# Optimization experiments

Measured on AMD Instinct MI355X. Metric: run time of the kernel, lower is better.

The kernel has to match this reference:

```python
import jax, jax.numpy as jnp
import numpy as np
from jax import lax

# Conv3d(in_dim, in_dim, kernel=(1,3,3), padding=(0,1,1)) == per-time-slice 3x3 conv mixing channels

def _conv3d(x, w, b):
    # x: [B, C, T, W, H], w: [O, I, 1, 3, 3], b: [O]
    y = lax.conv_general_dilated(
        x, w,
        window_strides=(1, 1, 1),
        padding=[(0, 0), (1, 1), (1, 1)],
        dimension_numbers=("NCDHW", "OIDHW", "NCDHW"),
    )
    return y + b[None, :, None, None, None]


def setup_inputs() -> dict:
    key = jax.random.key(0)
    ks = jax.random.split(key, 8)
    B, C, T, W, H = 8, 64, 16, 64, 64
    fan = C * 1 * 3 * 3
    bound = 1.0 / np.sqrt(fan)  # torch Conv3d default init range
    x = jax.random.normal(ks[0], (B, C, T, W, H), dtype=jnp.float32)
    wq = jax.random.uniform(ks[1], (C, C, 1, 3, 3), jnp.float32, -bound, bound)
    wk = jax.random.uniform(ks[2], (C, C, 1, 3, 3), jnp.float32, -bound, bound)
    wv = jax.random.uniform(ks[3], (C, C, 1, 3, 3), jnp.float32, -bound, bound)
    bq = jax.random.uniform(ks[4], (C,), jnp.float32, -bound, bound)
    bk = jax.random.uniform(ks[5], (C,), jnp.float32, -bound, bound)
    bv = jax.random.uniform(ks[6], (C,), jnp.float32, -bound, bound)
    # torch init is gamma=0 (identity output); use nonzero so reference exercises the full path
    gamma = jax.random.normal(ks[7], (1,), dtype=jnp.float32) * 0.1
    return {"x": x, "wq": wq, "wk": wk, "wv": wv,
            "bq": bq, "bk": bk, "bv": bv, "gamma": gamma}


def reference(x, wq, wk, wv, bq, bk, bv, gamma):
    B, C, T, W, H = x.shape
    WH = W * H
    q = _conv3d(x, wq, bq).reshape(B, C, T, WH)
    k = _conv3d(x, wk, bk).reshape(B, C, T, WH)
    v = _conv3d(x, wv, bv).reshape(B, C, T, WH)
    # Original: (q[...,:,None] @ k[...,None,:]) @ v[...,:,None]  -> rank-1 energy, no softmax.
    # Exact reassociation: out_i = q_i * sum_j(k_j * v_j), avoiding the [WH, WH] matrix.
    s = jnp.sum(k * v, axis=-1, keepdims=True)  # [B, C, T, 1]
    out = (q * s).reshape(B, C, T, W, H)
    return gamma[0] * out + x
```

## Files before the change

### kernel.cpp

```cpp
#include <hip/hip_runtime.h>
#include <hip/hip_bf16.h>
#include <stdint.h>

typedef __attribute__((ext_vector_type(8))) short bf16x8;
typedef __attribute__((ext_vector_type(4))) float f32x4v;
typedef __attribute__((ext_vector_type(16))) float f32x16;

#define CH_STRIDE 65536

__device__ __forceinline__ uint16_t f2bf(float f) {
  uint32_t u = __builtin_bit_cast(uint32_t, f);
  u = (u + 0x7FFFu + ((u >> 16) & 1u)) >> 16;
  return (uint16_t)u;
}
__device__ __forceinline__ float bf2f(uint32_t b) {
  return __builtin_bit_cast(float, b << 16);
}
__device__ __forceinline__ uint16_t cvt_bf(float f) {
  return __builtin_bit_cast(uint16_t, __float2bfloat16(f));
}

#define MFMA32(a, b, c) __builtin_amdgcn_mfma_f32_32x32x16_bf16(a, b, c, 0, 0, 0)
#define LGKM0 asm volatile("s_waitcnt lgkmcnt(0)" ::: "memory")
#define BAR __builtin_amdgcn_s_barrier()
#define SCHED0 __builtin_amdgcn_sched_barrier(0)

#define LDSX6  (6 * 8 * 66 * 16)
#define LDSX10 (10 * 8 * 66 * 16)

__device__ __forceinline__ uint32_t swz(uint32_t b) {
  return b ^ (((b >> 7) & 7u) << 4);
}

__device__ __forceinline__ bf16x8 ldx(const uint8_t* ldsx, int row, int oct, int ci) {
  return *(const bf16x8*)(ldsx + swz((uint32_t)((row * 8 + oct) * 66 + ci) * 16u));
}

__device__ __forceinline__ void stage_unit(uint8_t* ldsx, const float* xs, int w0, int u) {
  int row = u >> 7, oct = (u >> 4) & 7, g = u & 15;
  int w = w0 - 1 + row;
  uint32_t base = (uint32_t)((row * 8 + oct) * 66 + 4 * g + 1) * 16u;
  if ((unsigned)w < 64u) {
    const float* p = xs + (size_t)(oct * 8) * CH_STRIDE + w * 64 + 4 * g;
    f32x4v v[8];
    #pragma unroll
    for (int j = 0; j < 8; ++j) v[j] = *(const f32x4v*)(p + (size_t)j * CH_STRIDE);
    #pragma unroll
    for (int c = 0; c < 4; ++c) {
      bf16x8 frag;
      #pragma unroll
      for (int q = 0; q < 4; ++q) {
        frag[2 * q]     = (short)cvt_bf(v[2 * q][c]);
        frag[2 * q + 1] = (short)cvt_bf(v[2 * q + 1][c]);
      }
      *(bf16x8*)(ldsx + swz(base + (uint32_t)c * 16u)) = frag;
    }
  } else {
    bf16x8 z = {};
    #pragma unroll
    for (int c = 0; c < 4; ++c)
      *(bf16x8*)(ldsx + swz(base + (uint32_t)c * 16u)) = z;
  }
}
__device__ __forceinline__ void stage_halo(uint8_t* ldsx, int tid, int nrow) {
  if (tid < nrow * 16) {
    int row = tid >> 4, rem = tid & 15;
    int oct = rem >> 1, side = rem & 1;
    bf16x8 z = {};
    *(bf16x8*)(ldsx + swz((uint32_t)((row * 8 + oct) * 66 + side * 65) * 16u)) = z;
  }
}
__device__ __forceinline__ void stage_x256(uint8_t* ldsx, const float* xs, int w0, int tid) {
  stage_halo(ldsx, tid, 6);
  #pragma unroll
  for (int k = 0; k < 3; ++k) stage_unit(ldsx, xs, w0, tid + k * 256);
}
__device__ __forceinline__ void stage_x1024(uint8_t* ldsx, const float* xs, int w0, int tid) {
  stage_halo(ldsx, tid, 10);
  stage_unit(ldsx, xs, w0, tid);
  if (tid < 256) stage_unit(ldsx, xs, w0, 1024 + tid);
}

__device__ __forceinline__ bf16x8 ldw_kv(const uint8_t* ldsw, int oct, int rowloc) {
  return *(const bf16x8*)(ldsw + (uint32_t)(oct * 128 + rowloc) * 16u);
}
__device__ __forceinline__ bf16x8 ldw_q(const uint8_t* ldsw, int oct, int row) {
  return *(const bf16x8*)(ldsw + (uint32_t)(oct * 64 + row) * 16u);
}
__device__ __forceinline__ void ldw_g_q(bf16x8* r, const uint16_t* wq, int tap, int tid) {
  #pragma unroll
  for (int k = 0; k < 2; ++k)
    r[k] = *(const bf16x8*)(wq + ((size_t)tap * 512 + tid + k * 256) * 8);
}
__device__ __forceinline__ void stw_q(uint8_t* ldsw, const bf16x8* r, int tid) {
  #pragma unroll
  for (int k = 0; k < 2; ++k)
    *(bf16x8*)(ldsw + (uint32_t)(tid + k * 256) * 16u) = r[k];
}

__global__ void prep_weights(const float* __restrict__ wq, const float* __restrict__ wk,
                             const float* __restrict__ wv, uint16_t* __restrict__ wout) {
  int i = blockIdx.x * 256 + threadIdx.x;
  if (i >= 110592) return;
  if (i < 36864) {
    int tap = i >> 12, oct = (i >> 9) & 7, row = (i >> 3) & 63, j = i & 7;
    wout[i] = f2bf(wq[(row * 64 + oct * 8 + j) * 9 + tap]);
  } else {
    int m = i - 36864;
    int tap = m >> 13, oct = (m >> 10) & 7, rl = (m >> 3) & 127, j = m & 7;
    const float* src = (rl < 64) ? wk : wv;
    wout[i] = f2bf(src[((rl & 63) * 64 + oct * 8 + j) * 9 + tap]);
  }
}

__global__ __launch_bounds__(1024, 4) void kv_s_kernel(
    const float* __restrict__ x, const uint16_t* __restrict__ wkv,
    const float* __restrict__ bk, const float* __restrict__ bv,
    float* __restrict__ s_out) {
  extern __shared__ uint8_t lds[];
  uint8_t* ldsx = lds;
  uint8_t* ldswA = lds + LDSX10;
  uint8_t* ldswB = lds + LDSX10 + 16384;
  const int tid = threadIdx.x;
  const int l = tid & 63;
  const int wid = tid >> 6;
  const int ng = wid & 7, mg = wid >> 3;
  int bid = (int)(blockIdx.x & 7) * 128 + (int)(blockIdx.x >> 3);
  const int rg = bid & 7, slice = bid >> 3;
  const int b = slice >> 4, t = slice & 15;
  const int w0 = rg * 8;
  const float* xs = x + ((size_t)b * 1024 + t) * 4096;
  const int lm = l & 31, lh = l >> 5;

  stage_x1024(ldsx, xs, w0, tid);
  bf16x8 r_pref;
  r_pref = *(const bf16x8*)(wkv + (size_t)tid * 8);
  *(bf16x8*)(ldswA + (uint32_t)tid * 16u) = r_pref;
  r_pref = *(const bf16x8*)(wkv + ((size_t)1024 + tid) * 8);
  SCHED0; LGKM0; BAR; SCHED0;

  f32x16 accK[2], accV[2];
  #pragma unroll
  for (int nt = 0; nt < 2; ++nt)
    #pragma unroll
    for (int q = 0; q < 16; ++q) { accK[nt][q] = 0.f; accV[nt][q] = 0.f; }

  #pragma unroll
  for (int tap = 0; tap < 9; ++tap) {
    const int dy = tap / 3, dx = tap % 3;
    const uint8_t* bufc = (tap & 1) ? ldswB : ldswA;
    uint8_t* bufn = (tap & 1) ? ldswA : ldswB;
    int oct0 = lh;
    bf16x8 aK = ldw_kv(bufc, oct0, mg * 32 + lm);
    bf16x8 aV = ldw_kv(bufc, oct0, 64 + mg * 32 + lm);
    bf16x8 b0 = ldx(ldsx, ng + dy, oct0, lm + dx);
    bf16x8 b1 = ldx(ldsx, ng + dy, oct0, 32 + lm + dx);
    if (tap < 8) {
      *(bf16x8*)(bufn + (uint32_t)tid * 16u) = r_pref;
      if (tap < 7)
        r_pref = *(const bf16x8*)(wkv + ((size_t)(tap + 2) * 1024 + tid) * 8);
    }
    __builtin_amdgcn_s_setprio(1);
    accK[0] = MFMA32(aK, b0, accK[0]);
    accK[1] = MFMA32(aK, b1, accK[1]);
    accV[0] = MFMA32(aV, b0, accV[0]);
    accV[1] = MFMA32(aV, b1, accV[1]);
    #pragma unroll
    for (int s = 1; s < 4; ++s) {
      int oct = s * 2 + lh;
      aK = ldw_kv(bufc, oct, mg * 32 + lm);
      aV = ldw_kv(bufc, oct, 64 + mg * 32 + lm);
      b0 = ldx(ldsx, ng + dy, oct, lm + dx);
      b1 = ldx(ldsx, ng + dy, oct, 32 + lm + dx);
      accK[0] = MFMA32(aK, b0, accK[0]);
      accK[1] = MFMA32(aK, b1, accK[1]);
      accV[0] = MFMA32(aV, b0, accV[0]);
      accV[1] = MFMA32(aV, b1, accV[1]);
    }
    __builtin_amdgcn_s_setprio(0);
    SCHED0; LGKM0; BAR; SCHED0;
  }

  __syncthreads();
  float* red = (float*)lds;
  #pragma unroll
  for (int q = 0; q < 16; ++q) {
    int cl = (q & 3) + 8 * (q >> 2) + 4 * lh;
    int c = mg * 32 + cl;
    float bkc = bk[c], bvc = bv[c];
    float p = (accK[0][q] + bkc) * (accV[0][q] + bvc)
            + (accK[1][q] + bkc) * (accV[1][q] + bvc);
    red[c * 260 + ng * 32 + lm] = p;
  }
  __syncthreads();
  if (tid < 64) {
    const f32x4v* rp = (const f32x4v*)(red + tid * 260);
    f32x4v a4 = {0.f, 0.f, 0.f, 0.f};
    #pragma unroll
    for (int j = 0; j < 64; ++j) a4 += rp[j];
    atomicAdd(s_out + (b * 16 + t) * 64 + tid, a4[0] + a4[1] + a4[2] + a4[3]);
  }
}

__global__ __launch_bounds__(256, 2) void q_out_kernel(
    const float* __restrict__ x, const uint16_t* __restrict__ wq,
    const float* __restrict__ bq, const float* __restrict__ s_in,
    const float* __restrict__ gamma, float* __restrict__ out) {
  extern __shared__ uint8_t lds[];
  uint8_t* ldsx = lds;
  uint8_t* ldsw = lds + LDSX6;
  const int tid = threadIdx.x;
  const int l = tid & 63, ng = tid >> 6;
  int bid = (int)(blockIdx.x & 7) * 256 + (int)(blockIdx.x >> 3);
  const int rg = bid & 15, slice = bid >> 4;
  const int b = slice >> 4, t = slice & 15;
  const int w0 = rg * 4;
  const float* xs = x + ((size_t)b * 1024 + t) * 4096;
  const int lm = l & 31, lh = l >> 5;

  stage_x256(ldsx, xs, w0, tid);
  bf16x8 r[2];
  ldw_g_q(r, wq, 0, tid);
  stw_q(ldsw, r, tid);
  ldw_g_q(r, wq, 1, tid);
  SCHED0; LGKM0; BAR; SCHED0;

  f32x16 acc[2][2];
  #pragma unroll
  for (int mt = 0; mt < 2; ++mt)
    #pragma unroll
    for (int nt = 0; nt < 2; ++nt)
      #pragma unroll
      for (int q = 0; q < 16; ++q) acc[mt][nt][q] = 0.f;

  #pragma unroll
  for (int tap = 0; tap < 9; ++tap) {
    const int dy = tap / 3, dx = tap % 3;
    __builtin_amdgcn_s_setprio(1);
    #pragma unroll
    for (int s = 0; s < 4; ++s) {
      int oct = s * 2 + lh;
      bf16x8 a0 = ldw_q(ldsw, oct, lm);
      bf16x8 a1 = ldw_q(ldsw, oct, 32 + lm);
      bf16x8 b0 = ldx(ldsx, ng + dy, oct, lm + dx);
      bf16x8 b1 = ldx(ldsx, ng + dy, oct, 32 + lm + dx);
      acc[0][0] = MFMA32(a0, b0, acc[0][0]);
      acc[0][1] = MFMA32(a0, b1, acc[0][1]);
      acc[1][0] = MFMA32(a1, b0, acc[1][0]);
      acc[1][1] = MFMA32(a1, b1, acc[1][1]);
    }
    __builtin_amdgcn_s_setprio(0);
    if (tap < 8) {
      SCHED0; BAR;
      stw_q(ldsw, r, tid);
      if (tap < 7) ldw_g_q(r, wq, tap + 2, tid);
      SCHED0; LGKM0; BAR; SCHED0;
    }
  }

  float g = gamma[0];
  const float* sb = s_in + (b * 16 + t) * 64;
  int w = w0 + ng;
  #pragma unroll
  for (int mt = 0; mt < 2; ++mt) {
    #pragma unroll
    for (int q = 0; q < 16; ++q) {
      int cl = (q & 3) + 8 * (q >> 2) + 4 * lh;
      int c  = mt * 32 + cl;
      float qb = bq[c], sc = sb[c];
      #pragma unroll
      for (int nt = 0; nt < 2; ++nt) {
        int h = nt * 32 + lm;
        uint32_t xb = (uint32_t)(((ng + 1) * 8 + (c >> 3)) * 66 + (h + 1)) * 16u
                    + (uint32_t)(c & 7) * 2u;
        float xv = bf2f(*(const uint16_t*)(ldsx + swz(xb)));
        size_t idx = ((size_t)(b * 64 + c) * 16 + t) * 4096 + (size_t)w * 64 + h;
        out[idx] = g * (acc[mt][nt][q] + qb) * sc + xv;
      }
    }
  }
}

extern "C" void kernel_launch(void* const* d_in, const int* in_sizes, int n_in,
                              void* d_out, int out_size, void* d_ws, size_t ws_size,
                              hipStream_t stream) {
  const float* x   = (const float*)d_in[0];
  const float* wq  = (const float*)d_in[1];
  const float* wk  = (const float*)d_in[2];
  const float* wv  = (const float*)d_in[3];
  const float* bq  = (const float*)d_in[4];
  const float* bk  = (const float*)d_in[5];
  const float* bv  = (const float*)d_in[6];
  const float* gam = (const float*)d_in[7];

  uint16_t* wbf = (uint16_t*)d_ws;
  float* sbuf   = (float*)((uint8_t*)d_ws + 221184);

  hipMemsetAsync(sbuf, 0, 8 * 16 * 64 * sizeof(float), stream);
  prep_weights<<<(110592 + 255) / 256, 256, 0, stream>>>(wq, wk, wv, wbf);
  kv_s_kernel<<<1024, 1024, LDSX10 + 32768, stream>>>(x, wbf + 36864, bk, bv, sbuf);
  q_out_kernel<<<2048, 256, LDSX6 + 8192, stream>>>(x, wbf, bq, sbuf, gam, (float*)d_out);
}
```

Before: 156.2 us.

## Pre-transpose x into padded bf16 channel-interleaved layout shared by both conv kernels

Adds a transpose_x kernel that converts x once into a bf16, halo-padded, channel-octet-interleaved layout in workspace. Both the KV and Q conv kernels then stage their input tiles with straight 16-byte copies instead of each doing strided fp32 loads and bf16 conversion, which halves the bytes they read and removes duplicated conversion work. The LDS swizzle is dropped because the staged layout is now a linear copy, and the reduction stride changes to 261. The cost is an extra pass that writes and rereads a roughly 71 MB buffer, plus possible LDS bank conflicts now that there is no swizzle.

```diff
diff --git a/kernel.cpp b/kernel.cpp
--- a/kernel.cpp
+++ b/kernel.cpp
@@ -7,6 +7,8 @@
 typedef __attribute__((ext_vector_type(16))) float f32x16;
 
 #define CH_STRIDE 65536
+#define ROW_B 8448
+#define SLICE_B 557568
 
 __device__ __forceinline__ uint16_t f2bf(float f) {
   uint32_t u = __builtin_bit_cast(uint32_t, f);
@@ -28,57 +30,8 @@
 #define LDSX6  (6 * 8 * 66 * 16)
 #define LDSX10 (10 * 8 * 66 * 16)
 
-__device__ __forceinline__ uint32_t swz(uint32_t b) {
-  return b ^ (((b >> 7) & 7u) << 4);
-}
-
 __device__ __forceinline__ bf16x8 ldx(const uint8_t* ldsx, int row, int oct, int ci) {
-  return *(const bf16x8*)(ldsx + swz((uint32_t)((row * 8 + oct) * 66 + ci) * 16u));
-}
-
-__device__ __forceinline__ void stage_unit(uint8_t* ldsx, const float* xs, int w0, int u) {
-  int row = u >> 7, oct = (u >> 4) & 7, g = u & 15;
-  int w = w0 - 1 + row;
-  uint32_t base = (uint32_t)((row * 8 + oct) * 66 + 4 * g + 1) * 16u;
-  if ((unsigned)w < 64u) {
-    const float* p = xs + (size_t)(oct * 8) * CH_STRIDE + w * 64 + 4 * g;
-    f32x4v v[8];
-    #pragma unroll
-    for (int j = 0; j < 8; ++j) v[j] = *(const f32x4v*)(p + (size_t)j * CH_STRIDE);
-    #pragma unroll
-    for (int c = 0; c < 4; ++c) {
-      bf16x8 frag;
-      #pragma unroll
-      for (int q = 0; q < 4; ++q) {
-        frag[2 * q]     = (short)cvt_bf(v[2 * q][c]);
-        frag[2 * q + 1] = (short)cvt_bf(v[2 * q + 1][c]);
-      }
-      *(bf16x8*)(ldsx + swz(base + (uint32_t)c * 16u)) = frag;
-    }
-  } else {
-    bf16x8 z = {};
-    #pragma unroll
-    for (int c = 0; c < 4; ++c)
-      *(bf16x8*)(ldsx + swz(base + (uint32_t)c * 16u)) = z;
-  }
-}
-__device__ __forceinline__ void stage_halo(uint8_t* ldsx, int tid, int nrow) {
-  if (tid < nrow * 16) {
-    int row = tid >> 4, rem = tid & 15;
-    int oct = rem >> 1, side = rem & 1;
-    bf16x8 z = {};
-    *(bf16x8*)(ldsx + swz((uint32_t)((row * 8 + oct) * 66 + side * 65) * 16u)) = z;
-  }
-}
-__device__ __forceinline__ void stage_x256(uint8_t* ldsx, const float* xs, int w0, int tid) {
-  stage_halo(ldsx, tid, 6);
-  #pragma unroll
-  for (int k = 0; k < 3; ++k) stage_unit(ldsx, xs, w0, tid + k * 256);
-}
-__device__ __forceinline__ void stage_x1024(uint8_t* ldsx, const float* xs, int w0, int tid) {
-  stage_halo(ldsx, tid, 10);
-  stage_unit(ldsx, xs, w0, tid);
-  if (tid < 256) stage_unit(ldsx, xs, w0, 1024 + tid);
+  return *(const bf16x8*)(ldsx + (uint32_t)((row * 8 + oct) * 66 + ci) * 16u);
 }
 
 __device__ __forceinline__ bf16x8 ldw_kv(const uint8_t* ldsw, int oct, int rowloc) {
@@ -113,8 +66,61 @@
   }
 }
 
+__global__ __launch_bounds__(256, 4) void transpose_x(const float* __restrict__ x,
+                                                      uint8_t* __restrict__ xT) {
+  __shared__ uint8_t lds[4 * 8 * 66 * 16];
+  const int tid = threadIdx.x;
+  const int bid = blockIdx.x;
+  const int gg = bid % 17, slice = bid / 17;
+  const int b = slice >> 4, t = slice & 15;
+  const int r0 = gg * 4;
+  const int nrow = (gg == 16) ? 2 : 4;
+  const float* xs = x + ((size_t)b * 1024 + t) * 4096;
+
+  if (tid < nrow * 16) {
+    int row = tid >> 4, rem = tid & 15;
+    int oct = rem >> 1, side = rem & 1;
+    bf16x8 z = {};
+    *(bf16x8*)(lds + (uint32_t)((row * 8 + oct) * 66 + side * 65) * 16u) = z;
+  }
+  #pragma unroll
+  for (int k = 0; k < 2; ++k) {
+    int u = tid + k * 256;
+    if (u < nrow * 128) {
+      int row = u >> 7, oct = (u >> 4) & 7, g = u & 15;
+      int w = r0 + row - 1;
+      uint32_t base = (uint32_t)((row * 8 + oct) * 66 + 4 * g + 1) * 16u;
+      if ((unsigned)w < 64u) {
+        const float* p = xs + (size_t)(oct * 8) * CH_STRIDE + w * 64 + 4 * g;
+        f32x4v v[8];
+        #pragma unroll
+        for (int j = 0; j < 8; ++j) v[j] = *(const f32x4v*)(p + (size_t)j * CH_STRIDE);
+        #pragma unroll
+        for (int c = 0; c < 4; ++c) {
+          bf16x8 frag;
+          #pragma unroll
+          for (int q = 0; q < 4; ++q) {
+            frag[2 * q]     = (short)cvt_bf(v[2 * q][c]);
+            frag[2 * q + 1] = (short)cvt_bf(v[2 * q + 1][c]);
+          }
+          *(bf16x8*)(lds + base + (uint32_t)c * 16u) = frag;
+        }
+      } else {
+        bf16x8 z = {};
+        #pragma unroll
+        for (int c = 0; c < 4; ++c)
+          *(bf16x8*)(lds + base + (uint32_t)c * 16u) = z;
+      }
+    }
+  }
+  __syncthreads();
+  uint8_t* dst = xT + (size_t)slice * SLICE_B + (size_t)r0 * 528 * 16;
+  for (int i = tid; i < nrow * 528; i += 256)
+    *(bf16x8*)(dst + (uint32_t)i * 16u) = *(const bf16x8*)(lds + (uint32_t)i * 16u);
+}
+
 __global__ __launch_bounds__(1024, 4) void kv_s_kernel(
-    const float* __restrict__ x, const uint16_t* __restrict__ wkv,
+    const uint8_t* __restrict__ xT, const uint16_t* __restrict__ wkv,
     const float* __restrict__ bk, const float* __restrict__ bv,
     float* __restrict__ s_out) {
   extern __shared__ uint8_t lds[];
@@ -129,10 +135,15 @@
   const int rg = bid & 7, slice = bid >> 3;
   const int b = slice >> 4, t = slice & 15;
   const int w0 = rg * 8;
-  const float* xs = x + ((size_t)b * 1024 + t) * 4096;
   const int lm = l & 31, lh = l >> 5;
 
-  stage_x1024(ldsx, xs, w0, tid);
+  const uint8_t* gx = xT + (size_t)slice * SLICE_B + (size_t)w0 * ROW_B;
+  #pragma unroll
+  for (int k = 0; k < 6; ++k) {
+    int idx = tid + k * 1024;
+    if (idx < 5280)
+      *(bf16x8*)(ldsx + (uint32_t)idx * 16u) = *(const bf16x8*)(gx + (uint32_t)idx * 16u);
+  }
   bf16x8 r_pref;
   r_pref = *(const bf16x8*)(wkv + (size_t)tid * 8);
   *(bf16x8*)(ldswA + (uint32_t)tid * 16u) = r_pref;
@@ -190,20 +201,20 @@
     float bkc = bk[c], bvc = bv[c];
     float p = (accK[0][q] + bkc) * (accV[0][q] + bvc)
             + (accK[1][q] + bkc) * (accV[1][q] + bvc);
-    red[c * 260 + ng * 32 + lm] = p;
+    red[c * 261 + ng * 32 + lm] = p;
   }
   __syncthreads();
   if (tid < 64) {
-    const f32x4v* rp = (const f32x4v*)(red + tid * 260);
+    const float* rp = red + tid * 261;
     f32x4v a4 = {0.f, 0.f, 0.f, 0.f};
     #pragma unroll
-    for (int j = 0; j < 64; ++j) a4 += rp[j];
+    for (int j = 0; j < 64; ++j) a4 += *(const f32x4v*)(rp + j * 4);
     atomicAdd(s_out + (b * 16 + t) * 64 + tid, a4[0] + a4[1] + a4[2] + a4[3]);
   }
 }
 
 __global__ __launch_bounds__(256, 2) void q_out_kernel(
-    const float* __restrict__ x, const uint16_t* __restrict__ wq,
+    const uint8_t* __restrict__ xT, const uint16_t* __restrict__ wq,
     const float* __restrict__ bq, const float* __restrict__ s_in,
     const float* __restrict__ gamma, float* __restrict__ out) {
   extern __shared__ uint8_t lds[];
@@ -215,10 +226,15 @@
   const int rg = bid & 15, slice = bid >> 4;
   const int b = slice >> 4, t = slice & 15;
   const int w0 = rg * 4;
-  const float* xs = x + ((size_t)b * 1024 + t) * 4096;
   const int lm = l & 31, lh = l >> 5;
 
-  stage_x256(ldsx, xs, w0, tid);
+  const uint8_t* gx = xT + (size_t)slice * SLICE_B + (size_t)w0 * ROW_B;
+  #pragma unroll
+  for (int k = 0; k < 13; ++k) {
+    int idx = tid + k * 256;
+    if (idx < 3168)
+      *(bf16x8*)(ldsx + (uint32_t)idx * 16u) = *(const bf16x8*)(gx + (uint32_t)idx * 16u);
+  }
   bf16x8 r[2];
   ldw_g_q(r, wq, 0, tid);
   stw_q(ldsw, r, tid);
@@ -273,7 +289,7 @@
         int h = nt * 32 + lm;
         uint32_t xb = (uint32_t)(((ng + 1) * 8 + (c >> 3)) * 66 + (h + 1)) * 16u
                     + (uint32_t)(c & 7) * 2u;
-        float xv = bf2f(*(const uint16_t*)(ldsx + swz(xb)));
+        float xv = bf2f(*(const uint16_t*)(ldsx + xb));
         size_t idx = ((size_t)(b * 64 + c) * 16 + t) * 4096 + (size_t)w * 64 + h;
         out[idx] = g * (acc[mt][nt][q] + qb) * sc + xv;
       }
@@ -295,9 +311,12 @@
 
   uint16_t* wbf = (uint16_t*)d_ws;
   float* sbuf   = (float*)((uint8_t*)d_ws + 221184);
+  uint8_t* xT   = (uint8_t*)d_ws + 1048576;
+  if (ws_size < (size_t)1048576 + 128 * (size_t)SLICE_B) return;
 
   hipMemsetAsync(sbuf, 0, 8 * 16 * 64 * sizeof(float), stream);
   prep_weights<<<(110592 + 255) / 256, 256, 0, stream>>>(wq, wk, wv, wbf);
-  kv_s_kernel<<<1024, 1024, LDSX10 + 32768, stream>>>(x, wbf + 36864, bk, bv, sbuf);
-  q_out_kernel<<<2048, 256, LDSX6 + 8192, stream>>>(x, wbf, bq, sbuf, gam, (float*)d_out);
-}
+  transpose_x<<<128 * 17, 256, 0, stream>>>(x, xT);
+  kv_s_kernel<<<1024, 1024, LDSX10 + 32768, stream>>>(xT, wbf + 36864, bk, bv, sbuf);
+  q_out_kernel<<<2048, 256, LDSX6 + 8192, stream>>>(xT, wbf, bq, sbuf, gam, (float*)d_out);
+}
```

After: 181.8 us. 1.16x slower.
